# Optimization experiments

Hardware: AMD Instinct MI355X
Metric: run time of the kernel (lower is better)

The kernel has to match this reference:

```python
import jax, jax.numpy as jnp
import numpy as np

N_CELLS = 131072
IN_D, HID_D, OUT_D = 64, 128, 64


def setup_inputs() -> dict:
    key = jax.random.key(0)
    ks = jax.random.split(key, 16)
    rn = lambda k, shape, s=1.0: jax.random.normal(k, shape, dtype=jnp.float32) * s
    return {
        "x": rn(ks[0], (1, IN_D)),
        "hiddens": rn(ks[1], (N_CELLS, HID_D), 0.1),
        # engine_a: Linear(192->128), Linear(128->64)  (torch weight layout [out,in])
        "W1a": rn(ks[2], (128, IN_D + HID_D), 0.1), "b1a": rn(ks[3], (128,), 0.1),
        "W2a": rn(ks[4], (OUT_D, 128), 0.1), "b2a": rn(ks[5], (OUT_D,), 0.1),
        # engine_g: same shapes
        "W1g": rn(ks[6], (128, IN_D + HID_D), 0.1), "b1g": rn(ks[7], (128,), 0.1),
        "W2g": rn(ks[8], (OUT_D, 128), 0.1), "b2g": rn(ks[9], (OUT_D,), 0.1),
        # GRUCell(input=OUT_D+1, hidden=HID_D)
        "Wih": rn(ks[10], (3 * HID_D, OUT_D + 1), 0.1), "Whh": rn(ks[11], (3 * HID_D, HID_D), 0.1),
        "bih": rn(ks[12], (3 * HID_D,), 0.1), "bhh": rn(ks[13], (3 * HID_D,), 0.1),
        # output_head: Linear(OUT_D -> IN_D)
        "Wo": rn(ks[14], (IN_D, OUT_D), 0.1), "bo": rn(ks[15], (IN_D,), 0.1),
        "step": 6,
    }


def gru_cell(inp, h, Wih, Whh, bih, bhh):
    gi = inp @ Wih.T + bih          # [N, 3H]
    gh = h @ Whh.T + bhh            # [N, 3H]
    ir, iz, i_n = jnp.split(gi, 3, axis=-1)
    hr, hz, h_n = jnp.split(gh, 3, axis=-1)
    r = jax.nn.sigmoid(ir + hr)
    z = jax.nn.sigmoid(iz + hz)
    n = jnp.tanh(i_n + r * h_n)
    return (1.0 - z) * n + z * h


def faction_sync(h, nf=8, sync=0.15, debate=0.15, step=0):
    n, d = h.shape
    nf = min(nf, n // 2)
    if nf < 2:
        return h
    fs = n // nf
    hf = h[: nf * fs].reshape(nf, fs, d)
    fm = hf.mean(axis=1, keepdims=True)             # per-faction mean
    hf = (1.0 - sync) * hf + sync * fm
    if step > 5:
        ops = hf.mean(axis=1)                       # [nf, d]
        go = ops.mean(axis=0)                       # [d] global opinion
        dc = max(1, fs // 4)
        hf = hf.at[:, :dc].set((1.0 - debate) * hf[:, :dc] + debate * go)
    return h.at[: nf * fs].set(hf.reshape(nf * fs, d))


def reference(x, hiddens, W1a, b1a, W2a, b2a, W1g, b1g, W2g, b2g,
              Wih, Whh, bih, bhh, Wo, bo, step):
    N = hiddens.shape[0]
    # all cells share the same x; batch the per-cell loop
    c = jnp.concatenate([jnp.broadcast_to(x, (N, x.shape[-1])), hiddens], axis=-1)  # [N,192]
    a = jax.nn.relu(c @ W1a.T + b1a) @ W2a.T + b2a   # [N, OUT_D]
    g = jax.nn.relu(c @ W1g.T + b1g) @ W2g.T + b2g   # [N, OUT_D]
    out = a - g                                      # [N, OUT_D]
    t = jnp.mean(out ** 2, axis=-1)                  # [N] per-cell tension
    # GRU inputs are detached in the original
    gru_in = jax.lax.stop_gradient(jnp.concatenate([out, t[:, None]], axis=-1))  # [N, OUT_D+1]
    new_h = gru_cell(gru_in, hiddens, Wih, Whh, bih, bhh)
    new_h = jax.lax.stop_gradient(new_h)             # .detach() on stacked hiddens
    new_h = faction_sync(new_h, step=int(step))
    # softmax weights built from .item() scalars -> constants w.r.t. grad
    w = jax.nn.softmax(jax.lax.stop_gradient(t))     # [N]
    combined = w @ out                               # [OUT_D]
    pred = (combined @ Wo.T + bo)[None, :]           # [1, IN_D]
    return pred, t.mean(), new_h
```

## Files before the change

kernel.cpp:

```cpp
#include <hip/hip_runtime.h>
#include <math.h>

#define NCELLS 131072
#define IND 64
#define HD 128
#define OUTD 64
#define NF 8
#define FS 16384
#define DC 4096
#define TB 64
#define NBLK (NCELLS/TB)
#define NTH 512
#define NREP 4

typedef __bf16 bf16x8 __attribute__((ext_vector_type(8)));
typedef float f32x4 __attribute__((ext_vector_type(4)));
typedef unsigned short us8 __attribute__((ext_vector_type(8)));

#define MFMA(a,b,c) __builtin_amdgcn_mfma_f32_16x16x32_bf16(a,b,c,0,0,0)

#define WS_W1H 0
#define WS_W2F 32768
#define WS_WIH 49152
#define WS_WHH 73728
#define WS_U_TOTAL 122880
#define WF_B1   0
#define WF_B2   256
#define WF_WT   320
#define WF_FSUM 704
#define WF_WSUM 4800
#define WF_SE   5056
#define WF_TS   5060
#define WF_TOTAL 5064
#define WS_NH_OFF 266240

#define L_SC    0
#define L_SH1   8704
#define L_SOF_F 4352
#define L_SOB   17408
#define L_ST_F  11008
#define L_SE_F  11072
#define L_WSCR_F 11136
#define L_TOT   25600

__device__ __forceinline__ unsigned short f2bf(float f) {
    unsigned u = __builtin_bit_cast(unsigned, f);
    return (unsigned short)((u + 0x7FFFu + ((u >> 16) & 1u)) >> 16);
}
__device__ __forceinline__ float bf2f(unsigned short h) {
    return __builtin_bit_cast(float, (unsigned)h << 16);
}
__device__ __forceinline__ bf16x8 ld8(const unsigned short* p) {
    return __builtin_bit_cast(bf16x8, *(const us8*)p);
}
__device__ __forceinline__ float sigm(float v) {
    return __builtin_amdgcn_rcpf(1.f + __builtin_amdgcn_exp2f(-1.44269504f * v));
}
__device__ __forceinline__ float tanh_fast(float v) {
    return 1.f - 2.f * __builtin_amdgcn_rcpf(1.f + __builtin_amdgcn_exp2f(2.88539008f * v));
}

__global__ __launch_bounds__(256) void convert_kernel(
    const float* __restrict__ x,
    const float* __restrict__ W1a, const float* __restrict__ b1a,
    const float* __restrict__ W2a, const float* __restrict__ b2a,
    const float* __restrict__ W1g, const float* __restrict__ b1g,
    const float* __restrict__ W2g, const float* __restrict__ b2g,
    const float* __restrict__ Wih, const float* __restrict__ Whh,
    unsigned short* __restrict__ wsu, float* __restrict__ wsf)
{
    int i = blockIdx.x * 256 + threadIdx.x;
    if (i < 32768) {
        int frag = i >> 9, r = i & 511;
        int lane = r >> 3, e = r & 7;
        int col = (frag >> 2)*16 + (lane & 15);
        int k   = (frag & 3)*32 + (lane >> 4)*8 + e;
        float v = (col < 128) ? W1a[col*192 + 64 + k] : W1g[(col-128)*192 + 64 + k];
        wsu[WS_W1H + i] = f2bf(v); return;
    }
    int j = i - 32768;
    if (j < 16384) {
        int frag = j >> 9, r = j & 511;
        int lane = r >> 3, e = r & 7;
        int col = (frag >> 3)*16 + (lane & 15);
        int k   = (frag & 7)*32 + (lane >> 4)*8 + e;
        float v = (k < 128) ? W2a[col*128 + k] : -W2g[col*128 + (k-128)];
        wsu[WS_W2F + j] = f2bf(v); return;
    }
    j -= 16384;
    if (j < 24576) {
        int frag = j >> 9, r = j & 511;
        int lane = r >> 3, e = r & 7;
        int col = (frag >> 1)*16 + (lane & 15);
        int k   = (frag & 1)*32 + (lane >> 4)*8 + e;
        wsu[WS_WIH + j] = f2bf(Wih[col*65 + k]); return;
    }
    j -= 24576;
    if (j < 49152) {
        int frag = j >> 9, r = j & 511;
        int lane = r >> 3, e = r & 7;
        int col = (frag >> 2)*16 + (lane & 15);
        int k   = (frag & 3)*32 + (lane >> 4)*8 + e;
        wsu[WS_WHH + j] = f2bf(Whh[col*128 + k]); return;
    }
    j -= 49152;
    if (j < 256) {
        const float* wr = (j < 128) ? (W1a + j*192) : (W1g + (size_t)(j-128)*192);
        float base = (j < 128) ? b1a[j] : b1g[j-128];
        float dot = 0.f;
        #pragma unroll 8
        for (int k = 0; k < 64; ++k) dot += x[k] * wr[k];
        wsf[WF_B1 + j] = base + dot; return;
    }
    j -= 256;
    if (j < 64)  { wsf[WF_B2 + j] = b2a[j] - b2g[j]; return; }
    j -= 64;
    if (j < 384) { wsf[WF_WT + j] = Wih[j*65 + 64]; return; }
}

__global__ __launch_bounds__(NTH, 4) void fused_cell_kernel(
    const float* __restrict__ hiddens,
    const float* __restrict__ bih, const float* __restrict__ bhh,
    const unsigned short* __restrict__ wsu, const float* __restrict__ wsf,
    float* __restrict__ newh, float* __restrict__ fsum,
    float* __restrict__ wsum, float* __restrict__ sumexp, float* __restrict__ tsum)
{
    __shared__ __align__(16) unsigned short sm[L_TOT];
    float* smf = (float*)sm;

    const int tid = threadIdx.x;
    const int cell0 = blockIdx.x * TB;
    const int w = tid >> 6, lane = tid & 63;
    const int q = lane >> 4, cL = lane & 15;
    const int rep = blockIdx.x & (NREP-1);

    for (int idx = tid; idx < TB*(HD/4); idx += NTH) {
        int c = idx >> 5, k4 = idx & 31;
        float4 v = ((const float4*)hiddens)[(size_t)(cell0+c)*(HD/4) + k4];
        unsigned p0 = (unsigned)f2bf(v.x) | ((unsigned)f2bf(v.y) << 16);
        unsigned p1 = (unsigned)f2bf(v.z) | ((unsigned)f2bf(v.w) << 16);
        *(unsigned*)&sm[L_SC + c*136 + k4*4]     = p0;
        *(unsigned*)&sm[L_SC + c*136 + k4*4 + 2] = p1;
    }
    __syncthreads();

    #pragma unroll
    for (int ct = 0; ct < 2; ++ct) {
        const int col = w*32 + ct*16 + cL;
        const float bias = wsf[WF_B1 + col];
        f32x4 acc[4];
        #pragma unroll
        for (int m = 0; m < 4; ++m) acc[m] = (f32x4){bias,bias,bias,bias};
        const unsigned short* wp = wsu + WS_W1H + (w*2 + ct)*4*512 + lane*8;
        #pragma unroll
        for (int k = 0; k < 4; ++k) {
            bf16x8 B = ld8(wp + k*512);
            #pragma unroll
            for (int m = 0; m < 4; ++m) {
                bf16x8 A = ld8(&sm[L_SC + (m*16+cL)*136 + k*32 + q*8]);
                acc[m] = MFMA(A, B, acc[m]);
            }
        }
        #pragma unroll
        for (int m = 0; m < 4; ++m)
            #pragma unroll
            for (int r = 0; r < 4; ++r)
                sm[L_SH1 + (m*16+q*4+r)*264 + col] = f2bf(fmaxf(acc[m][r], 0.f));
    }
    __syncthreads();

    f32x4 o0, o1;
    {
        const int col = (w & 3)*16 + cL;
        const int Mt0 = (w >> 2)*2, Mt1 = Mt0 + 1;
        const float bias = wsf[WF_B2 + col];
        o0 = (f32x4){bias,bias,bias,bias}; o1 = o0;
        const unsigned short* wp = wsu + WS_W2F + (w & 3)*8*512 + lane*8;
        #pragma unroll
        for (int k = 0; k < 8; ++k) {
            bf16x8 B  = ld8(wp + k*512);
            bf16x8 A0 = ld8(&sm[L_SH1 + (Mt0*16+cL)*264 + k*32 + q*8]);
            o0 = MFMA(A0, B, o0);
            bf16x8 A1 = ld8(&sm[L_SH1 + (Mt1*16+cL)*264 + k*32 + q*8]);
            o1 = MFMA(A1, B, o1);
        }
    }
    __syncthreads();

    {
        const int col = (w & 3)*16 + cL;
        const int Mt0 = (w >> 2)*2, Mt1 = Mt0 + 1;
        #pragma unroll
        for (int r = 0; r < 4; ++r) {
            int r0 = Mt0*16 + q*4 + r, r1 = Mt1*16 + q*4 + r;
            smf[L_SOF_F + r0*68 + col] = o0[r];
            sm [L_SOB   + r0*72 + col] = f2bf(o0[r]);
            smf[L_SOF_F + r1*68 + col] = o1[r];
            sm [L_SOB   + r1*72 + col] = f2bf(o1[r]);
        }
    }
    __syncthreads();

    {
        const int c = tid >> 3, g = tid & 7;
        f32x4 a = *(const f32x4*)&smf[L_SOF_F + c*68 + g*8];
        f32x4 b = *(const f32x4*)&smf[L_SOF_F + c*68 + g*8 + 4];
        float s = a[0]*a[0] + a[1]*a[1] + a[2]*a[2] + a[3]*a[3]
                + b[0]*b[0] + b[1]*b[1] + b[2]*b[2] + b[3]*b[3];
        s += __shfl_xor(s, 1);
        s += __shfl_xor(s, 2);
        s += __shfl_xor(s, 4);
        if (g == 0) {
            float t = s * (1.0f/OUTD);
            smf[L_ST_F + c] = t;
            smf[L_SE_F + c] = __builtin_amdgcn_exp2f(t * 1.44269504f);
        }
    }
    __syncthreads();

    const int fidx = (int)(blockIdx.x >> 8);
    {
        const int j = w*16 + cL;
        const float bR = bih[j]      + bhh[j];
        const float bZ = bih[HD+j]   + bhh[HD+j];
        const float bI = bih[2*HD+j];
        const float bH = bhh[2*HD+j];
        const float wtR = wsf[WF_WT + j];
        const float wtZ = wsf[WF_WT + HD + j];
        const float wtI = wsf[WF_WT + 2*HD + j];
        const unsigned short* wiB = wsu + WS_WIH + lane*8;
        const unsigned short* whB = wsu + WS_WHH + lane*8;
        float colsum = 0.f;
        #pragma unroll
        for (int half = 0; half < 2; ++half) {
            const int Mt0 = half*2, Mt1 = Mt0 + 1;
            f32x4 R0 = {bR,bR,bR,bR}, R1 = R0;
            f32x4 Z0 = {bZ,bZ,bZ,bZ}, Z1 = Z0;
            f32x4 I0 = {bI,bI,bI,bI}, I1 = I0;
            f32x4 H0 = {bH,bH,bH,bH}, H1 = H0;
            #pragma unroll
            for (int k = 0; k < 2; ++k) {
                bf16x8 Br = ld8(wiB + ((w     )*2 + k)*512);
                bf16x8 Bz = ld8(wiB + ((8  + w)*2 + k)*512);
                bf16x8 Bi = ld8(wiB + ((16 + w)*2 + k)*512);
                bf16x8 A0 = ld8(&sm[L_SOB + (Mt0*16+cL)*72 + k*32 + q*8]);
                bf16x8 A1 = ld8(&sm[L_SOB + (Mt1*16+cL)*72 + k*32 + q*8]);
                R0 = MFMA(A0, Br, R0); R1 = MFMA(A1, Br, R1);
                Z0 = MFMA(A0, Bz, Z0); Z1 = MFMA(A1, Bz, Z1);
                I0 = MFMA(A0, Bi, I0); I1 = MFMA(A1, Bi, I1);
            }
            #pragma unroll
            for (int k = 0; k < 4; ++k) {
                bf16x8 Br = ld8(whB + ((w     )*4 + k)*512);
                bf16x8 Bz = ld8(whB + ((8  + w)*4 + k)*512);
                bf16x8 Bn = ld8(whB + ((16 + w)*4 + k)*512);
                bf16x8 A0 = ld8(&sm[L_SC + (Mt0*16+cL)*136 + k*32 + q*8]);
                bf16x8 A1 = ld8(&sm[L_SC + (Mt1*16+cL)*136 + k*32 + q*8]);
                R0 = MFMA(A0, Br, R0); R1 = MFMA(A1, Br, R1);
                Z0 = MFMA(A0, Bz, Z0); Z1 = MFMA(A1, Bz, Z1);
                H0 = MFMA(A0, Bn, H0); H1 = MFMA(A1, Bn, H1);
            }
            #pragma unroll
            for (int r = 0; r < 4; ++r) {
                const int row = Mt0*16 + q*4 + r;
                const float tv = smf[L_ST_F + row];
                const float rr = sigm(R0[r] + tv*wtR);
                const float zz = sigm(Z0[r] + tv*wtZ);
                const float nn = tanh_fast(I0[r] + tv*wtI + rr*H0[r]);
                const float hold = bf2f(sm[L_SC + row*136 + j]);
                const float hv = (1.f - zz)*nn + zz*hold;
                newh[(size_t)(cell0+row)*HD + j] = hv;
                colsum += hv;
            }
            #pragma unroll
            for (int r = 0; r < 4; ++r) {
                const int row = Mt1*16 + q*4 + r;
                const float tv = smf[L_ST_F + row];
                const float rr = sigm(R1[r] + tv*wtR);
                const float zz = sigm(Z1[r] + tv*wtZ);
                const float nn = tanh_fast(I1[r] + tv*wtI + rr*H1[r]);
                const float hold = bf2f(sm[L_SC + row*136 + j]);
                const float hv = (1.f - zz)*nn + zz*hold;
                newh[(size_t)(cell0+row)*HD + j] = hv;
                colsum += hv;
            }
        }
        colsum += __shfl_xor(colsum, 16);
        colsum += __shfl_xor(colsum, 32);
        if (q == 0) unsafeAtomicAdd(&fsum[(rep*NF + fidx)*HD + j], colsum);
    }

    {
        const int col = tid & 63, cg = tid >> 6;
        float wacc = 0.f;
        #pragma unroll
        for (int c8 = 0; c8 < 8; ++c8) {
            const int c = cg*8 + c8;
            wacc += smf[L_SE_F + c] * smf[L_SOF_F + c*68 + col];
        }
        smf[L_WSCR_F + cg*64 + col] = wacc;
    }
    __syncthreads();
    if (tid < 64) {
        float wacc = 0.f;
        #pragma unroll
        for (int g = 0; g < 8; ++g) wacc += smf[L_WSCR_F + g*64 + tid];
        unsafeAtomicAdd(&wsum[rep*64 + tid], wacc);
        float e = smf[L_SE_F + tid];
        float t = smf[L_ST_F + tid];
        #pragma unroll
        for (int d = 1; d < 64; d <<= 1) { e += __shfl_xor(e, d); t += __shfl_xor(t, d); }
        if (tid == 0) { unsafeAtomicAdd(&sumexp[rep], e); unsafeAtomicAdd(&tsum[rep], t); }
    }
}

#define TBF 64
__global__ __launch_bounds__(256) void faction_kernel(
    const float* __restrict__ src, float* __restrict__ dst,
    const float* __restrict__ fsum, const int* __restrict__ step,
    const float* __restrict__ Wo, const float* __restrict__ bo,
    const float* __restrict__ wsum, const float* __restrict__ sumexp,
    const float* __restrict__ tsum, float* __restrict__ d_out)
{
    __shared__ float bnon[HD], bdeb[HD];
    const int cell0 = blockIdx.x * TBF;
    const int f = blockIdx.x >> 8;
    if (threadIdx.x < HD) {
        const int jc = threadIdx.x;
        float s = 0.f, fm_s = 0.f;
        #pragma unroll
        for (int rr = 0; rr < NREP; ++rr) {
            #pragma unroll
            for (int ff = 0; ff < NF; ++ff) s += fsum[(rr*NF+ff)*HD + jc];
            fm_s += fsum[(rr*NF+f)*HD + jc];
        }
        const float go = s * (1.0f/NCELLS);
        const float fm = fm_s * (1.0f/FS);
        bnon[jc] = 0.15f*fm;
        bdeb[jc] = 0.1275f*fm + 0.15f*go;
    }
    __syncthreads();
    const bool debate = (step[0] > 5) && ((cell0 & (FS-1)) < DC);
    const float a = debate ? 0.7225f : 0.85f;
    const float* brow = debate ? bdeb : bnon;
    const float* srow = src + (size_t)cell0*HD;
    float* drow = dst + (size_t)cell0*HD;
    if ((((uintptr_t)srow) & 15) == 0) {
        const float4* s4 = (const float4*)srow;
        #pragma unroll
        for (int i = 0; i < (TBF*HD)/(256*4); ++i) {
            const int idx4 = threadIdx.x + i*256;
            const int jb = (idx4 & 31)*4;
            float4 v = s4[idx4];
            float r0 = a*v.x + brow[jb];
            float r1 = a*v.y + brow[jb+1];
            float r2 = a*v.z + brow[jb+2];
            float r3 = a*v.w + brow[jb+3];
            float* dp = drow + (size_t)idx4*4;
            dp[0] = r0; dp[1] = r1; dp[2] = r2; dp[3] = r3;
        }
    } else {
        #pragma unroll
        for (int i = 0; i < (TBF*HD)/256; ++i) {
            const int idx = threadIdx.x + i*256;
            const int jb = idx & 127;
            drow[idx] = a*srow[idx] + brow[jb];
        }
    }
    if (blockIdx.x == 0 && threadIdx.x < OUTD) {
        const int i = threadIdx.x;
        float seT = 0.f;
        #pragma unroll
        for (int rr = 0; rr < NREP; ++rr) seT += sumexp[rr];
        const float inv = 1.0f / seT;
        const float* wr = Wo + (size_t)i*OUTD;
        float acc = bo[i];
        #pragma unroll 8
        for (int jj = 0; jj < OUTD; ++jj) {
            float wv = wsum[jj] + wsum[64+jj] + wsum[128+jj] + wsum[192+jj];
            acc += (wv*inv) * wr[jj];
        }
        d_out[i] = acc;
        if (i == 0) {
            float tT = 0.f;
            #pragma unroll
            for (int rr = 0; rr < NREP; ++rr) tT += tsum[rr];
            d_out[OUTD] = tT * (1.0f/NCELLS);
        }
    }
}

extern "C" void kernel_launch(void* const* d_in, const int* in_sizes, int n_in,
                              void* d_out, int out_size, void* d_ws, size_t ws_size,
                              hipStream_t stream)
{
    const float* x   = (const float*)d_in[0];
    const float* hid = (const float*)d_in[1];
    const float* W1a = (const float*)d_in[2];
    const float* b1a = (const float*)d_in[3];
    const float* W2a = (const float*)d_in[4];
    const float* b2a = (const float*)d_in[5];
    const float* W1g = (const float*)d_in[6];
    const float* b1g = (const float*)d_in[7];
    const float* W2g = (const float*)d_in[8];
    const float* b2g = (const float*)d_in[9];
    const float* Wih = (const float*)d_in[10];
    const float* Whh = (const float*)d_in[11];
    const float* bih = (const float*)d_in[12];
    const float* bhh = (const float*)d_in[13];
    const float* Wo  = (const float*)d_in[14];
    const float* bo  = (const float*)d_in[15];
    const int*  step = (const int*)d_in[16];

    float* out  = (float*)d_out;
    float* newh_out = out + (OUTD + 1);

    unsigned short* wsu = (unsigned short*)d_ws;
    float* wsf = (float*)(wsu + WS_U_TOTAL);
    float* fsum   = wsf + WF_FSUM;
    float* wsum   = wsf + WF_WSUM;
    float* sumexp = wsf + WF_SE;
    float* tsum   = wsf + WF_TS;

    const size_t need = (size_t)WS_NH_OFF + (size_t)NCELLS*HD*sizeof(float);
    float* nh_store = (ws_size >= need) ? (float*)((char*)d_ws + WS_NH_OFF) : newh_out;

    hipMemsetAsync(fsum, 0, (NREP*NF*HD + NREP*OUTD + 2*NREP)*sizeof(float), stream);

    convert_kernel<<<(123584 + 255)/256, 256, 0, stream>>>(
        x, W1a, b1a, W2a, b2a, W1g, b1g, W2g, b2g, Wih, Whh, wsu, wsf);

    fused_cell_kernel<<<NBLK, NTH, 0, stream>>>(
        hid, bih, bhh, wsu, wsf, nh_store, fsum, wsum, sumexp, tsum);

    faction_kernel<<<NCELLS/TBF, 256, 0, stream>>>(
        nh_store, newh_out, fsum, step, Wo, bo, wsum, sumexp, tsum, out);
}
```

Measured before the change: 237.9 us.

## Halve cell tile per block to 32 cells with 256 threads

Shrinks the main kernel's tile from 64 cells and 512 threads to 32 cells and 256 threads, doubling the block count and halving shared memory per block. Each wave now covers more output columns (four column tiles in layer 1, two hidden-column tiles in the GRU) across fewer rows, and the faction index shift and reductions are adjusted to match. The aim is better occupancy and load balance across CUs. In exchange, weight fragments are reloaded per smaller tile and atomics to the faction, weight and exp sums double.

```diff
diff --git a/kernel.cpp b/kernel.cpp
--- a/kernel.cpp
+++ b/kernel.cpp
@@ -8,9 +8,9 @@
 #define NF 8
 #define FS 16384
 #define DC 4096
-#define TB 64
+#define TB 32
 #define NBLK (NCELLS/TB)
-#define NTH 512
+#define NTH 256
 #define NREP 4
 
 typedef __bf16 bf16x8 __attribute__((ext_vector_type(8)));
@@ -35,13 +35,13 @@
 #define WS_NH_OFF 266240
 
 #define L_SC    0
-#define L_SH1   8704
-#define L_SOF_F 4352
-#define L_SOB   17408
-#define L_ST_F  11008
-#define L_SE_F  11072
-#define L_WSCR_F 11136
-#define L_TOT   25600
+#define L_SH1   4352
+#define L_SOF_F 2176
+#define L_SOB   8704
+#define L_ST_F  6400
+#define L_SE_F  6432
+#define L_WSCR_F 6464
+#define L_TOT   13440
 
 __device__ __forceinline__ unsigned short f2bf(float f) {
     unsigned u = __builtin_bit_cast(unsigned, f);
@@ -145,24 +145,24 @@
     __syncthreads();
 
     #pragma unroll
-    for (int ct = 0; ct < 2; ++ct) {
-        const int col = w*32 + ct*16 + cL;
+    for (int ct = 0; ct < 4; ++ct) {
+        const int col = w*64 + ct*16 + cL;
         const float bias = wsf[WF_B1 + col];
-        f32x4 acc[4];
-        #pragma unroll
-        for (int m = 0; m < 4; ++m) acc[m] = (f32x4){bias,bias,bias,bias};
-        const unsigned short* wp = wsu + WS_W1H + (w*2 + ct)*4*512 + lane*8;
+        f32x4 acc[2];
+        #pragma unroll
+        for (int m = 0; m < 2; ++m) acc[m] = (f32x4){bias,bias,bias,bias};
+        const unsigned short* wp = wsu + WS_W1H + (w*4 + ct)*4*512 + lane*8;
         #pragma unroll
         for (int k = 0; k < 4; ++k) {
             bf16x8 B = ld8(wp + k*512);
             #pragma unroll
-            for (int m = 0; m < 4; ++m) {
+            for (int m = 0; m < 2; ++m) {
                 bf16x8 A = ld8(&sm[L_SC + (m*16+cL)*136 + k*32 + q*8]);
                 acc[m] = MFMA(A, B, acc[m]);
             }
         }
         #pragma unroll
-        for (int m = 0; m < 4; ++m)
+        for (int m = 0; m < 2; ++m)
             #pragma unroll
             for (int r = 0; r < 4; ++r)
                 sm[L_SH1 + (m*16+q*4+r)*264 + col] = f2bf(fmaxf(acc[m][r], 0.f));
@@ -171,28 +171,26 @@
 
     f32x4 o0, o1;
     {
-        const int col = (w & 3)*16 + cL;
-        const int Mt0 = (w >> 2)*2, Mt1 = Mt0 + 1;
+        const int col = w*16 + cL;
         const float bias = wsf[WF_B2 + col];
         o0 = (f32x4){bias,bias,bias,bias}; o1 = o0;
-        const unsigned short* wp = wsu + WS_W2F + (w & 3)*8*512 + lane*8;
+        const unsigned short* wp = wsu + WS_W2F + w*8*512 + lane*8;
         #pragma unroll
         for (int k = 0; k < 8; ++k) {
             bf16x8 B  = ld8(wp + k*512);
-            bf16x8 A0 = ld8(&sm[L_SH1 + (Mt0*16+cL)*264 + k*32 + q*8]);
+            bf16x8 A0 = ld8(&sm[L_SH1 + (cL)*264 + k*32 + q*8]);
             o0 = MFMA(A0, B, o0);
-            bf16x8 A1 = ld8(&sm[L_SH1 + (Mt1*16+cL)*264 + k*32 + q*8]);
+            bf16x8 A1 = ld8(&sm[L_SH1 + (16+cL)*264 + k*32 + q*8]);
             o1 = MFMA(A1, B, o1);
         }
     }
     __syncthreads();
 
     {
-        const int col = (w & 3)*16 + cL;
-        const int Mt0 = (w >> 2)*2, Mt1 = Mt0 + 1;
+        const int col = w*16 + cL;
         #pragma unroll
         for (int r = 0; r < 4; ++r) {
-            int r0 = Mt0*16 + q*4 + r, r1 = Mt1*16 + q*4 + r;
+            int r0 = q*4 + r, r1 = 16 + q*4 + r;
             smf[L_SOF_F + r0*68 + col] = o0[r];
             sm [L_SOB   + r0*72 + col] = f2bf(o0[r]);
             smf[L_SOF_F + r1*68 + col] = o1[r];
@@ -218,51 +216,52 @@
     }
     __syncthreads();
 
-    const int fidx = (int)(blockIdx.x >> 8);
+    const int fidx = (int)(blockIdx.x >> 9);
     {
-        const int j = w*16 + cL;
-        const float bR = bih[j]      + bhh[j];
-        const float bZ = bih[HD+j]   + bhh[HD+j];
-        const float bI = bih[2*HD+j];
-        const float bH = bhh[2*HD+j];
-        const float wtR = wsf[WF_WT + j];
-        const float wtZ = wsf[WF_WT + HD + j];
-        const float wtI = wsf[WF_WT + 2*HD + j];
-        const unsigned short* wiB = wsu + WS_WIH + lane*8;
-        const unsigned short* whB = wsu + WS_WHH + lane*8;
-        float colsum = 0.f;
-        #pragma unroll
-        for (int half = 0; half < 2; ++half) {
-            const int Mt0 = half*2, Mt1 = Mt0 + 1;
+        float colsum;
+        #pragma unroll
+        for (int jt2 = 0; jt2 < 2; ++jt2) {
+            const int jt = jt2*4 + w;
+            const int j  = jt*16 + cL;
+            const float bR = bih[j]      + bhh[j];
+            const float bZ = bih[HD+j]   + bhh[HD+j];
+            const float bI = bih[2*HD+j];
+            const float bH = bhh[2*HD+j];
+            const float wtR = wsf[WF_WT + j];
+            const float wtZ = wsf[WF_WT + HD + j];
+            const float wtI = wsf[WF_WT + 2*HD + j];
+            const unsigned short* wiB = wsu + WS_WIH + lane*8;
+            const unsigned short* whB = wsu + WS_WHH + lane*8;
             f32x4 R0 = {bR,bR,bR,bR}, R1 = R0;
             f32x4 Z0 = {bZ,bZ,bZ,bZ}, Z1 = Z0;
             f32x4 I0 = {bI,bI,bI,bI}, I1 = I0;
             f32x4 H0 = {bH,bH,bH,bH}, H1 = H0;
             #pragma unroll
             for (int k = 0; k < 2; ++k) {
-                bf16x8 Br = ld8(wiB + ((w     )*2 + k)*512);
-                bf16x8 Bz = ld8(wiB + ((8  + w)*2 + k)*512);
-                bf16x8 Bi = ld8(wiB + ((16 + w)*2 + k)*512);
-                bf16x8 A0 = ld8(&sm[L_SOB + (Mt0*16+cL)*72 + k*32 + q*8]);
-                bf16x8 A1 = ld8(&sm[L_SOB + (Mt1*16+cL)*72 + k*32 + q*8]);
+                bf16x8 Br = ld8(wiB + ((     jt)*2 + k)*512);
+                bf16x8 Bz = ld8(wiB + (( 8 + jt)*2 + k)*512);
+                bf16x8 Bi = ld8(wiB + ((16 + jt)*2 + k)*512);
+                bf16x8 A0 = ld8(&sm[L_SOB + (cL)*72 + k*32 + q*8]);
+                bf16x8 A1 = ld8(&sm[L_SOB + (16+cL)*72 + k*32 + q*8]);
                 R0 = MFMA(A0, Br, R0); R1 = MFMA(A1, Br, R1);
                 Z0 = MFMA(A0, Bz, Z0); Z1 = MFMA(A1, Bz, Z1);
                 I0 = MFMA(A0, Bi, I0); I1 = MFMA(A1, Bi, I1);
             }
             #pragma unroll
             for (int k = 0; k < 4; ++k) {
-                bf16x8 Br = ld8(whB + ((w     )*4 + k)*512);
-                bf16x8 Bz = ld8(whB + ((8  + w)*4 + k)*512);
-                bf16x8 Bn = ld8(whB + ((16 + w)*4 + k)*512);
-                bf16x8 A0 = ld8(&sm[L_SC + (Mt0*16+cL)*136 + k*32 + q*8]);
-                bf16x8 A1 = ld8(&sm[L_SC + (Mt1*16+cL)*136 + k*32 + q*8]);
+                bf16x8 Br = ld8(whB + ((     jt)*4 + k)*512);
+                bf16x8 Bz = ld8(whB + (( 8 + jt)*4 + k)*512);
+                bf16x8 Bn = ld8(whB + ((16 + jt)*4 + k)*512);
+                bf16x8 A0 = ld8(&sm[L_SC + (cL)*136 + k*32 + q*8]);
+                bf16x8 A1 = ld8(&sm[L_SC + (16+cL)*136 + k*32 + q*8]);
                 R0 = MFMA(A0, Br, R0); R1 = MFMA(A1, Br, R1);
                 Z0 = MFMA(A0, Bz, Z0); Z1 = MFMA(A1, Bz, Z1);
                 H0 = MFMA(A0, Bn, H0); H1 = MFMA(A1, Bn, H1);
             }
+            colsum = 0.f;
             #pragma unroll
             for (int r = 0; r < 4; ++r) {
-                const int row = Mt0*16 + q*4 + r;
+                const int row = q*4 + r;
                 const float tv = smf[L_ST_F + row];
                 const float rr = sigm(R0[r] + tv*wtR);
                 const float zz = sigm(Z0[r] + tv*wtZ);
@@ -274,7 +273,7 @@
             }
             #pragma unroll
             for (int r = 0; r < 4; ++r) {
-                const int row = Mt1*16 + q*4 + r;
+                const int row = 16 + q*4 + r;
                 const float tv = smf[L_ST_F + row];
                 const float rr = sigm(R1[r] + tv*wtR);
                 const float zz = sigm(Z1[r] + tv*wtZ);
@@ -284,10 +283,10 @@
                 newh[(size_t)(cell0+row)*HD + j] = hv;
                 colsum += hv;
             }
-        }
-        colsum += __shfl_xor(colsum, 16);
-        colsum += __shfl_xor(colsum, 32);
-        if (q == 0) unsafeAtomicAdd(&fsum[(rep*NF + fidx)*HD + j], colsum);
+            colsum += __shfl_xor(colsum, 16);
+            colsum += __shfl_xor(colsum, 32);
+            if (q == 0) unsafeAtomicAdd(&fsum[(rep*NF + fidx)*HD + j], colsum);
+        }
     }
 
     {
@@ -304,12 +303,14 @@
     if (tid < 64) {
         float wacc = 0.f;
         #pragma unroll
-        for (int g = 0; g < 8; ++g) wacc += smf[L_WSCR_F + g*64 + tid];
+        for (int g = 0; g < 4; ++g) wacc += smf[L_WSCR_F + g*64 + tid];
         unsafeAtomicAdd(&wsum[rep*64 + tid], wacc);
+    }
+    if (tid < 32) {
         float e = smf[L_SE_F + tid];
         float t = smf[L_ST_F + tid];
         #pragma unroll
-        for (int d = 1; d < 64; d <<= 1) { e += __shfl_xor(e, d); t += __shfl_xor(t, d); }
+        for (int d = 1; d < 32; d <<= 1) { e += __shfl_xor(e, d); t += __shfl_xor(t, d); }
         if (tid == 0) { unsafeAtomicAdd(&sumexp[rep], e); unsafeAtomicAdd(&tsum[rep], t); }
     }
 }
```

Result: slower. 279.3 us (+17.4%).

## Prefetch MFMA weights into registers, merge GRU tiles, shift scratch layout for aligned stores

Applied to the files above, without the earlier changes.

The fused cell kernel now preloads the W1, W2 and Wih fragments into registers before the barriers, so their global loads overlap with the staging of hidden states. The two GRU halves are merged into one pass over all four M tiles, which loads each Whh fragment once instead of twice. The scratch newh buffer is stored shifted by three floats, so that the faction kernel, which writes into the output at offset 65 floats, can read aligned float4 and issue aligned float4 stores. This adds index arithmetic, handling for rows that straddle cells and factions, and higher register pressure that may reduce occupancy.

```diff
diff --git a/kernel.cpp b/kernel.cpp
--- a/kernel.cpp
+++ b/kernel.cpp
@@ -12,6 +12,7 @@
 #define NBLK (NCELLS/TB)
 #define NTH 512
 #define NREP 4
+#define NT (NCELLS*HD)
 
 typedef __bf16 bf16x8 __attribute__((ext_vector_type(8)));
 typedef float f32x4 __attribute__((ext_vector_type(4)));
@@ -123,7 +124,8 @@
     const float* __restrict__ bih, const float* __restrict__ bhh,
     const unsigned short* __restrict__ wsu, const float* __restrict__ wsf,
     float* __restrict__ newh, float* __restrict__ fsum,
-    float* __restrict__ wsum, float* __restrict__ sumexp, float* __restrict__ tsum)
+    float* __restrict__ wsum, float* __restrict__ sumexp, float* __restrict__ tsum,
+    int shifted)
 {
     __shared__ __align__(16) unsigned short sm[L_TOT];
     float* smf = (float*)sm;
@@ -133,6 +135,13 @@
     const int w = tid >> 6, lane = tid & 63;
     const int q = lane >> 4, cL = lane & 15;
     const int rep = blockIdx.x & (NREP-1);
+
+    bf16x8 pB1[8];
+    {
+        const unsigned short* wp = wsu + WS_W1H + (w*2)*4*512 + lane*8;
+        #pragma unroll
+        for (int k = 0; k < 8; ++k) pB1[k] = ld8(wp + k*512);
+    }
 
     for (int idx = tid; idx < TB*(HD/4); idx += NTH) {
         int c = idx >> 5, k4 = idx & 31;
@@ -144,6 +153,12 @@
     }
     __syncthreads();
 
+    bf16x8 pB2[8];
+    {
+        const unsigned short* wp = wsu + WS_W2F + (w & 3)*8*512 + lane*8;
+        #pragma unroll
+        for (int k = 0; k < 8; ++k) pB2[k] = ld8(wp + k*512);
+    }
     #pragma unroll
     for (int ct = 0; ct < 2; ++ct) {
         const int col = w*32 + ct*16 + cL;
@@ -151,10 +166,9 @@
         f32x4 acc[4];
         #pragma unroll
         for (int m = 0; m < 4; ++m) acc[m] = (f32x4){bias,bias,bias,bias};
-        const unsigned short* wp = wsu + WS_W1H + (w*2 + ct)*4*512 + lane*8;
         #pragma unroll
         for (int k = 0; k < 4; ++k) {
-            bf16x8 B = ld8(wp + k*512);
+            bf16x8 B = pB1[ct*4 + k];
             #pragma unroll
             for (int m = 0; m < 4; ++m) {
                 bf16x8 A = ld8(&sm[L_SC + (m*16+cL)*136 + k*32 + q*8]);
@@ -169,16 +183,24 @@
     }
     __syncthreads();
 
+    bf16x8 pGi[6];
+    {
+        const unsigned short* wiB = wsu + WS_WIH + lane*8;
+        #pragma unroll
+        for (int k = 0; k < 2; ++k) {
+            pGi[k]   = ld8(wiB + ((     w)*2 + k)*512);
+            pGi[2+k] = ld8(wiB + (( 8 + w)*2 + k)*512);
+            pGi[4+k] = ld8(wiB + ((16 + w)*2 + k)*512);
+        }
+    }
     f32x4 o0, o1;
     {
-        const int col = (w & 3)*16 + cL;
         const int Mt0 = (w >> 2)*2, Mt1 = Mt0 + 1;
-        const float bias = wsf[WF_B2 + col];
+        const float bias = wsf[WF_B2 + (w & 3)*16 + cL];
         o0 = (f32x4){bias,bias,bias,bias}; o1 = o0;
-        const unsigned short* wp = wsu + WS_W2F + (w & 3)*8*512 + lane*8;
         #pragma unroll
         for (int k = 0; k < 8; ++k) {
-            bf16x8 B  = ld8(wp + k*512);
+            bf16x8 B  = pB2[k];
             bf16x8 A0 = ld8(&sm[L_SH1 + (Mt0*16+cL)*264 + k*32 + q*8]);
             o0 = MFMA(A0, B, o0);
             bf16x8 A1 = ld8(&sm[L_SH1 + (Mt1*16+cL)*264 + k*32 + q*8]);
@@ -228,60 +250,54 @@
         const float wtR = wsf[WF_WT + j];
         const float wtZ = wsf[WF_WT + HD + j];
         const float wtI = wsf[WF_WT + 2*HD + j];
-        const unsigned short* wiB = wsu + WS_WIH + lane*8;
+        f32x4 R[4], Z[4], I[4], H[4];
+        #pragma unroll
+        for (int m = 0; m < 4; ++m) {
+            R[m] = (f32x4){bR,bR,bR,bR}; Z[m] = (f32x4){bZ,bZ,bZ,bZ};
+            I[m] = (f32x4){bI,bI,bI,bI}; H[m] = (f32x4){bH,bH,bH,bH};
+        }
+        #pragma unroll
+        for (int k = 0; k < 2; ++k) {
+            bf16x8 Br = pGi[k], Bz = pGi[2+k], Bi = pGi[4+k];
+            #pragma unroll
+            for (int m = 0; m < 4; ++m) {
+                bf16x8 A = ld8(&sm[L_SOB + (m*16+cL)*72 + k*32 + q*8]);
+                R[m] = MFMA(A, Br, R[m]);
+                Z[m] = MFMA(A, Bz, Z[m]);
+                I[m] = MFMA(A, Bi, I[m]);
+            }
+        }
         const unsigned short* whB = wsu + WS_WHH + lane*8;
+        #pragma unroll
+        for (int k = 0; k < 4; ++k) {
+            bf16x8 Br = ld8(whB + ((     w)*4 + k)*512);
+            bf16x8 Bz = ld8(whB + (( 8 + w)*4 + k)*512);
+            bf16x8 Bn = ld8(whB + ((16 + w)*4 + k)*512);
+            #pragma unroll
+            for (int m = 0; m < 4; ++m) {
+                bf16x8 A = ld8(&sm[L_SC + (m*16+cL)*136 + k*32 + q*8]);
+                R[m] = MFMA(A, Br, R[m]);
+                Z[m] = MFMA(A, Bz, Z[m]);
+                H[m] = MFMA(A, Bn, H[m]);
+            }
+        }
         float colsum = 0.f;
         #pragma unroll
-        for (int half = 0; half < 2; ++half) {
-            const int Mt0 = half*2, Mt1 = Mt0 + 1;
-            f32x4 R0 = {bR,bR,bR,bR}, R1 = R0;
-            f32x4 Z0 = {bZ,bZ,bZ,bZ}, Z1 = Z0;
-            f32x4 I0 = {bI,bI,bI,bI}, I1 = I0;
-            f32x4 H0 = {bH,bH,bH,bH}, H1 = H0;
-            #pragma unroll
-            for (int k = 0; k < 2; ++k) {
-                bf16x8 Br = ld8(wiB + ((w     )*2 + k)*512);
-                bf16x8 Bz = ld8(wiB + ((8  + w)*2 + k)*512);
-                bf16x8 Bi = ld8(wiB + ((16 + w)*2 + k)*512);
-                bf16x8 A0 = ld8(&sm[L_SOB + (Mt0*16+cL)*72 + k*32 + q*8]);
-                bf16x8 A1 = ld8(&sm[L_SOB + (Mt1*16+cL)*72 + k*32 + q*8]);
-                R0 = MFMA(A0, Br, R0); R1 = MFMA(A1, Br, R1);
-                Z0 = MFMA(A0, Bz, Z0); Z1 = MFMA(A1, Bz, Z1);
-                I0 = MFMA(A0, Bi, I0); I1 = MFMA(A1, Bi, I1);
-            }
-            #pragma unroll
-            for (int k = 0; k < 4; ++k) {
-                bf16x8 Br = ld8(whB + ((w     )*4 + k)*512);
-                bf16x8 Bz = ld8(whB + ((8  + w)*4 + k)*512);
-                bf16x8 Bn = ld8(whB + ((16 + w)*4 + k)*512);
-                bf16x8 A0 = ld8(&sm[L_SC + (Mt0*16+cL)*136 + k*32 + q*8]);
-                bf16x8 A1 = ld8(&sm[L_SC + (Mt1*16+cL)*136 + k*32 + q*8]);
-                R0 = MFMA(A0, Br, R0); R1 = MFMA(A1, Br, R1);
-                Z0 = MFMA(A0, Bz, Z0); Z1 = MFMA(A1, Bz, Z1);
-                H0 = MFMA(A0, Bn, H0); H1 = MFMA(A1, Bn, H1);
-            }
+        for (int m = 0; m < 4; ++m) {
             #pragma unroll
             for (int r = 0; r < 4; ++r) {
-                const int row = Mt0*16 + q*4 + r;
+                const int row = m*16 + q*4 + r;
                 const float tv = smf[L_ST_F + row];
-                const float rr = sigm(R0[r] + tv*wtR);
-                const float zz = sigm(Z0[r] + tv*wtZ);
-                const float nn = tanh_fast(I0[r] + tv*wtI + rr*H0[r]);
+                const float rr = sigm(R[m][r] + tv*wtR);
+                const float zz = sigm(Z[m][r] + tv*wtZ);
+                const float nn = tanh_fast(I[m][r] + tv*wtI + rr*H[m][r]);
                 const float hold = bf2f(sm[L_SC + row*136 + j]);
                 const float hv = (1.f - zz)*nn + zz*hold;
-                newh[(size_t)(cell0+row)*HD + j] = hv;
-                colsum += hv;
-            }
-            #pragma unroll
-            for (int r = 0; r < 4; ++r) {
-                const int row = Mt1*16 + q*4 + r;
-                const float tv = smf[L_ST_F + row];
-                const float rr = sigm(R1[r] + tv*wtR);
-                const float zz = sigm(Z1[r] + tv*wtZ);
-                const float nn = tanh_fast(I1[r] + tv*wtI + rr*H1[r]);
-                const float hold = bf2f(sm[L_SC + row*136 + j]);
-                const float hv = (1.f - zz)*nn + zz*hold;
-                newh[(size_t)(cell0+row)*HD + j] = hv;
+                int g = (cell0+row)*HD + j;
+                int s = g - 3;
+                if (g < 3) s = NT - 3 + g;
+                if (!shifted) s = g;
+                newh[s] = hv;
                 colsum += hv;
             }
         }
@@ -320,54 +336,84 @@
     const float* __restrict__ fsum, const int* __restrict__ step,
     const float* __restrict__ Wo, const float* __restrict__ bo,
     const float* __restrict__ wsum, const float* __restrict__ sumexp,
-    const float* __restrict__ tsum, float* __restrict__ d_out)
+    const float* __restrict__ tsum, float* __restrict__ d_out, int shifted)
 {
-    __shared__ float bnon[HD], bdeb[HD];
-    const int cell0 = blockIdx.x * TBF;
-    const int f = blockIdx.x >> 8;
-    if (threadIdx.x < HD) {
-        const int jc = threadIdx.x;
+    __shared__ float bnon[HD], bdeb[HD], bnon2[HD], bdeb2[HD];
+    const int b = blockIdx.x;
+    const int f = b >> 8;
+    const int fn = (f + 1 < NF) ? f + 1 : f;
+    {
+        const int jc = threadIdx.x & 127;
+        const int useF = (threadIdx.x < 128) ? f : fn;
         float s = 0.f, fm_s = 0.f;
         #pragma unroll
         for (int rr = 0; rr < NREP; ++rr) {
             #pragma unroll
             for (int ff = 0; ff < NF; ++ff) s += fsum[(rr*NF+ff)*HD + jc];
-            fm_s += fsum[(rr*NF+f)*HD + jc];
+            fm_s += fsum[(rr*NF+useF)*HD + jc];
         }
         const float go = s * (1.0f/NCELLS);
         const float fm = fm_s * (1.0f/FS);
-        bnon[jc] = 0.15f*fm;
-        bdeb[jc] = 0.1275f*fm + 0.15f*go;
-    }
-    __syncthreads();
-    const bool debate = (step[0] > 5) && ((cell0 & (FS-1)) < DC);
-    const float a = debate ? 0.7225f : 0.85f;
-    const float* brow = debate ? bdeb : bnon;
-    const float* srow = src + (size_t)cell0*HD;
-    float* drow = dst + (size_t)cell0*HD;
-    if ((((uintptr_t)srow) & 15) == 0) {
-        const float4* s4 = (const float4*)srow;
-        #pragma unroll
-        for (int i = 0; i < (TBF*HD)/(256*4); ++i) {
-            const int idx4 = threadIdx.x + i*256;
-            const int jb = (idx4 & 31)*4;
-            float4 v = s4[idx4];
-            float r0 = a*v.x + brow[jb];
-            float r1 = a*v.y + brow[jb+1];
-            float r2 = a*v.z + brow[jb+2];
-            float r3 = a*v.w + brow[jb+3];
-            float* dp = drow + (size_t)idx4*4;
-            dp[0] = r0; dp[1] = r1; dp[2] = r2; dp[3] = r3;
+        if (threadIdx.x < 128) { bnon[jc] = 0.15f*fm;  bdeb[jc] = 0.1275f*fm + 0.15f*go; }
+        else                   { bnon2[jc] = 0.15f*fm; bdeb2[jc] = 0.1275f*fm + 0.15f*go; }
+    }
+    __syncthreads();
+    const int sglob = (step[0] > 5) ? 1 : 0;
+
+    if (shifted) {
+        const int Fbase = b * 2048;
+        #pragma unroll
+        for (int it = 0; it < 8; ++it) {
+            const int F  = Fbase + threadIdx.x + it*256;
+            const int g0 = 4*F + 3;
+            float4 v = ((const float4*)src)[F];
+            const int c0 = g0 >> 7, j0 = g0 & 127;
+            const int d0 = sglob && ((c0 & (FS-1)) < DC);
+            const float a0 = d0 ? 0.7225f : 0.85f;
+            const float* br0 = d0 ? bdeb : bnon;
+            float r0 = a0*v.x + br0[j0], r1, r2, r3;
+            if (j0 != 127) {
+                r1 = a0*v.y + br0[j0+1];
+                r2 = a0*v.z + br0[j0+2];
+                r3 = a0*v.w + br0[j0+3];
+            } else {
+                const int c1 = c0 + 1;
+                const int d1 = sglob && ((c1 & (FS-1)) < DC);
+                const float a1 = d1 ? 0.7225f : 0.85f;
+                const bool nf2 = (c1 >> 14) != f;
+                const float* br1 = nf2 ? (d1 ? bdeb2 : bnon2) : (d1 ? bdeb : bnon);
+                r1 = a1*v.y + br1[0];
+                r2 = a1*v.z + br1[1];
+                r3 = a1*v.w + br1[2];
+            }
+            if (g0 + 3 < NT) {
+                float4 o = {r0, r1, r2, r3};
+                *(float4*)(dst + g0) = o;
+            } else {
+                dst[g0] = r0;
+            }
+        }
+        if (b == 0 && threadIdx.x < 3) {
+            const int g = threadIdx.x;
+            const float a0 = sglob ? 0.7225f : 0.85f;
+            const float* br0 = sglob ? bdeb : bnon;
+            dst[g] = a0 * src[NT - 3 + g] + br0[g];
         }
     } else {
+        const int cell0 = b * TBF;
+        const bool debate = sglob && ((cell0 & (FS-1)) < DC);
+        const float a = debate ? 0.7225f : 0.85f;
+        const float* brow = debate ? bdeb : bnon;
+        const float* srow = src + (size_t)cell0*HD;
+        float* drow = dst + (size_t)cell0*HD;
         #pragma unroll
         for (int i = 0; i < (TBF*HD)/256; ++i) {
             const int idx = threadIdx.x + i*256;
-            const int jb = idx & 127;
-            drow[idx] = a*srow[idx] + brow[jb];
-        }
-    }
-    if (blockIdx.x == 0 && threadIdx.x < OUTD) {
+            drow[idx] = a*srow[idx] + brow[idx & 127];
+        }
+    }
+
+    if (b == 0 && threadIdx.x < OUTD) {
         const int i = threadIdx.x;
         float seT = 0.f;
         #pragma unroll
@@ -422,8 +468,9 @@
     float* sumexp = wsf + WF_SE;
     float* tsum   = wsf + WF_TS;
 
-    const size_t need = (size_t)WS_NH_OFF + (size_t)NCELLS*HD*sizeof(float);
-    float* nh_store = (ws_size >= need) ? (float*)((char*)d_ws + WS_NH_OFF) : newh_out;
+    const size_t need = (size_t)WS_NH_OFF + (size_t)NT*sizeof(float);
+    const int shifted = (ws_size >= need) ? 1 : 0;
+    float* nh_store = shifted ? (float*)((char*)d_ws + WS_NH_OFF) : newh_out;
 
     hipMemsetAsync(fsum, 0, (NREP*NF*HD + NREP*OUTD + 2*NREP)*sizeof(float), stream);
 
@@ -431,8 +478,8 @@
         x, W1a, b1a, W2a, b2a, W1g, b1g, W2g, b2g, Wih, Whh, wsu, wsf);
 
     fused_cell_kernel<<<NBLK, NTH, 0, stream>>>(
-        hid, bih, bhh, wsu, wsf, nh_store, fsum, wsum, sumexp, tsum);
+        hid, bih, bhh, wsu, wsf, nh_store, fsum, wsum, sumexp, tsum, shifted);
 
     faction_kernel<<<NCELLS/TBF, 256, 0, stream>>>(
-        nh_store, newh_out, fsum, step, Wo, bo, wsum, sumexp, tsum, out);
-}
+        nh_store, newh_out, fsum, step, Wo, bo, wsum, sumexp, tsum, out, shifted);
+}
```

After: 231.0 us. 1.03x faster.
